# Kernel tuning notes

Hardware: AMD Instinct MI355X
Metric: run time of the kernel (lower is better)

Reference implementation:

```python
import jax, jax.numpy as jnp
import numpy as np

NUM_HEADS = 14
SCALE = 0.125  # fixed constant in the source, not 1/sqrt(head_dim)
PATCH = 14
DIM = 3 * PATCH * PATCH  # 588


def setup_inputs() -> dict:
    key = jax.random.key(0)
    k_x, k_cw, k_cb, k_qw, k_qb = jax.random.split(key, 5)
    B, C_in, H, W = 8, 3, 448, 448
    x = jax.random.normal(k_x, (B, C_in, H, W), dtype=jnp.float32)
    # Conv2d(in_channels=3, dim, kernel=patch, stride=patch), torch layout OIHW
    fan_in = C_in * PATCH * PATCH
    bound = 1.0 / np.sqrt(fan_in)
    conv_w = jax.random.uniform(k_cw, (DIM, C_in, PATCH, PATCH), jnp.float32, -bound, bound)
    conv_b = jax.random.uniform(k_cb, (DIM,), jnp.float32, -bound, bound)
    # Linear(dim, 3*dim): weight [out, in] torch layout
    lb = 1.0 / np.sqrt(DIM)
    qkv_w = jax.random.uniform(k_qw, (3 * DIM, DIM), jnp.float32, -lb, lb)
    qkv_b = jax.random.uniform(k_qb, (3 * DIM,), jnp.float32, -lb, lb)
    return {"x": x, "conv_w": conv_w, "conv_b": conv_b, "qkv_w": qkv_w, "qkv_b": qkv_b}


def reference(x, conv_w, conv_b, qkv_w, qkv_b):
    # Patch embedding: conv kernel==stride==patch  -> [B, DIM, H/p, W/p]
    y = jax.lax.conv_general_dilated(
        x, conv_w, window_strides=(PATCH, PATCH), padding="VALID",
        dimension_numbers=("NCHW", "OIHW", "NCHW"))
    y = y + conv_b[None, :, None, None]
    B = y.shape[0]
    # flatten(2).transpose(1, 2) -> [B, N, C]
    tokens = y.reshape(B, DIM, -1).transpose(0, 2, 1)
    N, C = tokens.shape[1], tokens.shape[2]
    hd = C // NUM_HEADS  # 42
    qkv = tokens @ qkv_w.T + qkv_b  # [B, N, 3C]
    qkv = qkv.reshape(B, N, 3, NUM_HEADS, hd).transpose(2, 0, 3, 1, 4)  # [3,B,H,N,hd]
    q, k, v = qkv[0], qkv[1], qkv[2]
    attn = jnp.einsum("bhnd,bhmd->bhnm", q, k) * SCALE  # [B,H,N,N]
    attn = jax.nn.softmax(attn, axis=-1)
    out = jnp.einsum("bhnm,bhmd->bhnd", attn, v)  # [B,H,N,hd]
    out = out.transpose(0, 2, 1, 3).reshape(B, N, C)  # [B,N,C]
    return out
```

## Files before the change

### kernel.cpp

```cpp
#include <hip/hip_runtime.h>

typedef unsigned short u16;
typedef unsigned int u32;
typedef unsigned long long u64;
typedef __attribute__((ext_vector_type(8))) short bf16x8;
typedef __attribute__((ext_vector_type(4))) float f32x4;

#define MTOK 8192
#define KP   640
#define CC   588
#define C3   1764
#define NH   14
#define SEQ  1024
#define HD   42
#define DP   64
#define DV   48
#define SC2f 0.18033688011112042f

static __device__ __forceinline__ u16 f2b(float f) {
  unsigned u = __builtin_bit_cast(unsigned, f);
  u = (u + 0x7FFFu + ((u >> 16) & 1u)) >> 16;
  return (u16)u;
}

static __device__ __forceinline__ void gl_lds16(const void* g, void* l) {
  auto gp = (const unsigned int __attribute__((address_space(1)))*)((unsigned long long)g);
  auto lp = (unsigned int __attribute__((address_space(3)))*)((unsigned long long)l);
  __builtin_amdgcn_global_load_lds(gp, lp, 16, 0, 0);
}

static __device__ __forceinline__ u32 pk2(float lo, float hi) {
  u32 a = __builtin_bit_cast(u32, lo) + 0x8000u;
  u32 b = __builtin_bit_cast(u32, hi) + 0x8000u;
  return __builtin_amdgcn_perm(b, a, 0x07060302u);
}

__global__ void im2col_k(const float* __restrict__ x, u16* __restrict__ A,
                         u16* __restrict__ vT, u16* __restrict__ kb) {
  int t = blockIdx.x;
  int b = t >> 10, pi = t & 1023, ph = pi >> 5, pw = pi & 31;
  const float* xb = x + (size_t)b * 3 * 448 * 448;
  for (int kk = threadIdx.x; kk < KP; kk += 256) {
    float v = 0.f;
    if (kk < CC) {
      int c = kk / 196, rem = kk - c * 196, i = rem / 14, j = rem - i * 14;
      v = xb[(size_t)(c * 448 + ph * 14 + i) * 448 + pw * 14 + j];
    }
    A[(size_t)t * KP + kk] = f2b(v);
  }
  if (t < 112) {
    u16* row = vT + ((size_t)(t * DV + HD)) * SEQ;
    for (int n = threadIdx.x; n < SEQ; n += 256) row[n] = 0x3F80;
    for (int n = threadIdx.x; n < SEQ; n += 256) {
      u64* p = (u64*)&kb[((size_t)t * SEQ + n) * DP + 40];
      p[0] = 0; p[1] = 0; p[2] = 0;
    }
  }
}

__global__ void padw_k(const float* __restrict__ wc, const float* __restrict__ wq,
                       u16* __restrict__ dc, u16* __restrict__ dq) {
  int r = blockIdx.x;
  const float* src; u16* dst; int R, rr;
  if (r < 640) { src = wc; dst = dc; R = CC; rr = r; }
  else         { src = wq; dst = dq; R = C3; rr = r - 640; }
  for (int c = threadIdx.x; c < KP; c += 256) {
    float v = (rr < R && c < CC) ? src[(size_t)rr * CC + c] : 0.f;
    dst[(size_t)rr * KP + c] = f2b(v);
  }
}

template <int MODE>
__global__ void __launch_bounds__(256, 2) gemm_k(
    const u16* __restrict__ A, const u16* __restrict__ Bt,
    const float* __restrict__ bias, u16* __restrict__ out0,
    u16* __restrict__ qb, u16* __restrict__ kb, u16* __restrict__ vb) {
  __shared__ alignas(16) u16 sA[128 * 64];
  __shared__ alignas(16) u16 sB[128 * 64];
  const int tid = threadIdx.x;
  const int wave = tid >> 6, lane = tid & 63, quad = lane >> 4, l16 = lane & 15;
  const int wi = wave >> 1, wj = wave & 1;
  const int m0 = blockIdx.x * 128, n0 = blockIdx.y * 128;
  const int rL = lane >> 3, scid = lane & 7;
  const f32x4 z4 = {0.f, 0.f, 0.f, 0.f};

  f32x4 acc[4][4];
#pragma unroll
  for (int i = 0; i < 4; i++)
#pragma unroll
    for (int j = 0; j < 4; j++) acc[i][j] = z4;

  for (int k0 = 0; k0 < KP; k0 += 64) {
    __syncthreads();
#pragma unroll
    for (int cc = wave; cc < 16; cc += 4) {
      int r = cc * 8 + rL;
      gl_lds16(A + ((size_t)(m0 + r) * KP + k0 + (scid ^ (r & 7)) * 8), &sA[cc * 512]);
    }
#pragma unroll
    for (int cc = wave; cc < 16; cc += 4) {
      int r = cc * 8 + rL;
      gl_lds16(Bt + ((size_t)(n0 + r) * KP + k0 + (scid ^ (r & 7)) * 8), &sB[cc * 512]);
    }
    __syncthreads();
#pragma unroll
    for (int ks = 0; ks < 2; ks++) {
      bf16x8 af[4], bfr[4];
#pragma unroll
      for (int i = 0; i < 4; i++) {
        int r = wi * 64 + i * 16 + l16;
        af[i] = *(const bf16x8*)&sA[r * 64 + (((ks * 4 + quad) ^ (r & 7)) * 8)];
      }
#pragma unroll
      for (int j = 0; j < 4; j++) {
        int r = wj * 64 + j * 16 + l16;
        bfr[j] = *(const bf16x8*)&sB[r * 64 + (((ks * 4 + quad) ^ (r & 7)) * 8)];
      }
#pragma unroll
      for (int i = 0; i < 4; i++)
#pragma unroll
        for (int j = 0; j < 4; j++)
          acc[i][j] = __builtin_amdgcn_mfma_f32_16x16x32_bf16(af[i], bfr[j], acc[i][j], 0, 0, 0);
    }
  }

  const int baser = wi * 64 + quad * 4;
  if (MODE == 0) {
#pragma unroll
    for (int j = 0; j < 4; j++) {
      int col = n0 + wj * 64 + j * 16 + l16;
      float bs = (col < CC) ? bias[col] : 0.f;
#pragma unroll
      for (int i = 0; i < 4; i++) {
        int row = m0 + baser + i * 16;
#pragma unroll
        for (int r = 0; r < 4; r++)
          out0[(size_t)(row + r) * KP + col] = f2b(acc[i][j][r] + bs);
      }
    }
  } else {
#pragma unroll
    for (int j = 0; j < 4; j++) {
      int col = n0 + wj * 64 + j * 16 + l16;
      if (col < C3) {
        float bs = bias[col];
        int which = col / CC;
        int rem = col - which * CC;
        int h = rem / HD;
        int d = rem - h * HD;
        if (which < 2) {
          u16* dst = (which == 0) ? qb : kb;
          float sc = (which == 0) ? SC2f : 1.0f;
#pragma unroll
          for (int i = 0; i < 4; i++) {
            int row = m0 + baser + i * 16;
#pragma unroll
            for (int r = 0; r < 4; r++) {
              int rw = row + r;
              int b = rw >> 10, n = rw & 1023;
              dst[((size_t)((b * NH + h) * SEQ + n)) * DP + d] = f2b((acc[i][j][r] + bs) * sc);
            }
          }
        } else {
#pragma unroll
          for (int i = 0; i < 4; i++) {
            int row = m0 + baser + i * 16;
            int b = row >> 10, n = row & 1023;
            u64 pk = (u64)f2b(acc[i][j][0] + bs) | ((u64)f2b(acc[i][j][1] + bs) << 16) |
                     ((u64)f2b(acc[i][j][2] + bs) << 32) | ((u64)f2b(acc[i][j][3] + bs) << 48);
            *(u64*)&vb[((size_t)((b * NH + h) * DV + d)) * SEQ + n] = pk;
          }
        }
      }
    }
  }
}

__global__ void __launch_bounds__(256) attn_k(
    const u16* __restrict__ qb, const u16* __restrict__ kb,
    const u16* __restrict__ vT, float* __restrict__ out) {
  __shared__ alignas(16) u16 sK[2][64 * 64];
  __shared__ alignas(16) u16 sV[2][DV * 64];
  __shared__ alignas(16) u16 sP[4][16 * 72];
  const int tid = threadIdx.x;
  const int wave = tid >> 6, lane = tid & 63, quad = lane >> 4, l16 = lane & 15;
  const int g = blockIdx.x;
  const int bh = (g & 7) * 14 + (g >> 7);
  const int qt = (g >> 3) & 15;
  const int q0 = qt * 64;
  const int rL = lane >> 3, scid = lane & 7;
  const f32x4 z4 = {0.f, 0.f, 0.f, 0.f};
  u16* sPw = sP[wave];

  bf16x8 aq0, aq1;
  {
    const u16* qrow = qb + ((size_t)(bh * SEQ + q0 + wave * 16 + l16)) * DP;
    aq0 = *(const bf16x8*)&qrow[quad * 8];
    aq1 = *(const bf16x8*)&qrow[32 + quad * 8];
  }
  f32x4 o[3] = {z4, z4, z4};

  const u16* kb0 = kb + (size_t)bh * SEQ * DP;
  const u16* vb0 = vT + (size_t)bh * DV * SEQ;

#define STAGE(bufi, m0_)                                                                    \
  {                                                                                         \
    _Pragma("unroll") for (int cc = wave; cc < 8; cc += 4) {                                \
      int r = cc * 8 + rL;                                                                  \
      gl_lds16(kb0 + ((size_t)((m0_) + r)) * DP + (scid ^ ((r >> 2) & 7)) * 8,              \
               &sK[bufi][cc * 512]);                                                        \
    }                                                                                       \
    _Pragma("unroll") for (int cc = wave; cc < 6; cc += 4) {                                \
      int d = cc * 8 + rL;                                                                  \
      gl_lds16(vb0 + (size_t)d * SEQ + (m0_) + (scid ^ (d & 7)) * 8, &sV[bufi][cc * 512]);  \
    }                                                                                       \
  }

  STAGE(0, 0);

  for (int kt = 0; kt < 16; kt++) {
    __syncthreads();
    if (kt < 15) STAGE((kt + 1) & 1, (kt + 1) * 64);
    const u16* sKb = sK[kt & 1];
    const u16* sVb = sV[kt & 1];
    bf16x8 bk[4][2];
#pragma unroll
    for (int j = 0; j < 4; j++) {
      int rr = 4 * l16 + j;
#pragma unroll
      for (int ks = 0; ks < 2; ks++)
        bk[j][ks] = *(const bf16x8*)&sKb[rr * 64 + (((ks * 4 + quad) ^ (l16 & 7)) * 8)];
    }
    f32x4 s[4];
#pragma unroll
    for (int j = 0; j < 4; j++) {
      f32x4 t = __builtin_amdgcn_mfma_f32_16x16x32_bf16(aq0, bk[j][0], z4, 0, 0, 0);
      s[j] = __builtin_amdgcn_mfma_f32_16x16x32_bf16(aq1, bk[j][1], t, 0, 0, 0);
    }
#pragma unroll
    for (int r = 0; r < 4; r++) {
      u32 d0 = pk2(__builtin_amdgcn_exp2f(s[0][r]), __builtin_amdgcn_exp2f(s[1][r]));
      u32 d1 = pk2(__builtin_amdgcn_exp2f(s[2][r]), __builtin_amdgcn_exp2f(s[3][r]));
      u32* dst = (u32*)&sPw[(quad * 4 + r) * 72 + l16 * 4];
      dst[0] = d0;
      dst[1] = d1;
    }
#pragma unroll
    for (int ks = 0; ks < 2; ks++) {
      bf16x8 ap = *(const bf16x8*)&sPw[l16 * 72 + ks * 32 + quad * 8];
#pragma unroll
      for (int j = 0; j < 3; j++) {
        int d = j * 16 + l16;
        bf16x8 bv = *(const bf16x8*)&sVb[d * 64 + (((ks * 4 + quad) ^ (d & 7)) * 8)];
        o[j] = __builtin_amdgcn_mfma_f32_16x16x32_bf16(ap, bv, o[j], 0, 0, 0);
      }
    }
  }
#undef STAGE

  const int b = bh / NH, h = bh - b * NH;
#pragma unroll
  for (int r = 0; r < 4; r++) {
    float ls = __shfl(o[2][r], (lane & 48) + 10, 64);
    float rc = 1.f / ls;
    int row = wave * 16 + quad * 4 + r;
    float* orow = out + ((size_t)(b * SEQ + q0 + row)) * CC + h * HD;
#pragma unroll
    for (int j = 0; j < 3; j++) {
      int d = j * 16 + l16;
      if (d < HD) orow[d] = o[j][r] * rc;
    }
  }
}

extern "C" void kernel_launch(void* const* d_in, const int* in_sizes, int n_in,
                              void* d_out, int out_size, void* d_ws, size_t ws_size,
                              hipStream_t stream) {
  (void)in_sizes; (void)n_in; (void)out_size; (void)ws_size;
  const float* x      = (const float*)d_in[0];
  const float* conv_w = (const float*)d_in[1];
  const float* conv_b = (const float*)d_in[2];
  const float* qkv_w  = (const float*)d_in[3];
  const float* qkv_b  = (const float*)d_in[4];
  float* out = (float*)d_out;

  char* ws = (char*)d_ws;
  size_t off = 0;
  u16* A      = (u16*)(ws + off); off += (size_t)MTOK * KP * 2;
  u16* Wc     = (u16*)(ws + off); off += (size_t)640 * KP * 2;
  u16* Wq     = (u16*)(ws + off); off += (size_t)1792 * KP * 2;
  u16* tokens = (u16*)(ws + off); off += (size_t)MTOK * KP * 2;
  u16* qbuf   = (u16*)(ws + off); off += (size_t)112 * SEQ * DP * 2;
  u16* kbuf   = (u16*)(ws + off); off += (size_t)112 * SEQ * DP * 2;
  u16* vTb    = (u16*)(ws + off); off += (size_t)112 * DV * SEQ * 2;

  im2col_k<<<MTOK, 256, 0, stream>>>(x, A, vTb, kbuf);
  padw_k<<<2432, 256, 0, stream>>>(conv_w, qkv_w, Wc, Wq);
  gemm_k<0><<<dim3(64, 5), 256, 0, stream>>>(A, Wc, conv_b, tokens, nullptr, nullptr, nullptr);
  gemm_k<1><<<dim3(64, 14), 256, 0, stream>>>(tokens, Wq, qkv_b, nullptr, qbuf, kbuf, vTb);
  attn_k<<<1792, 256, 0, stream>>>(qbuf, kbuf, vTb, out);
}
```

Measured before the change: 174.1 us.

## Fold patch-embedding conv weights into QKV projection to drop one token GEMM

Precomputes a fused weight Wf = Wq·Wc and fused bias (Wq·cb + qb) with a small weight-only GEMM, so the activations go through one GEMM instead of two (8192x640x640 conv GEMM eliminated). Also vectorizes the im2col bf16 packing, zeroes padding of q as well as k, and clamps the exp2 argument. The cost is an extra small weight GEMM each call and a different rounding path, since the fused weights are rounded to bf16 once rather than rounding the intermediate tokens.

New measurement: 188.3 us. 1.08x slower.

```diff
diff --git a/kernel.cpp b/kernel.cpp
--- a/kernel.cpp
+++ b/kernel.cpp
@@ -36,37 +36,51 @@
 }
 
 __global__ void im2col_k(const float* __restrict__ x, u16* __restrict__ A,
-                         u16* __restrict__ vT, u16* __restrict__ kb) {
+                         u16* __restrict__ vT, u16* __restrict__ qb, u16* __restrict__ kb) {
   int t = blockIdx.x;
   int b = t >> 10, pi = t & 1023, ph = pi >> 5, pw = pi & 31;
   const float* xb = x + (size_t)b * 3 * 448 * 448;
-  for (int kk = threadIdx.x; kk < KP; kk += 256) {
-    float v = 0.f;
+  u32* Arow = (u32*)(A + (size_t)t * KP);
+  for (int h = threadIdx.x; h < KP / 2; h += 256) {
+    int kk = h * 2;
+    u32 v = 0;
     if (kk < CC) {
       int c = kk / 196, rem = kk - c * 196, i = rem / 14, j = rem - i * 14;
-      v = xb[(size_t)(c * 448 + ph * 14 + i) * 448 + pw * 14 + j];
-    }
-    A[(size_t)t * KP + kk] = f2b(v);
+      const float* p = &xb[(size_t)(c * 448 + ph * 14 + i) * 448 + pw * 14 + j];
+      v = pk2(p[0], p[1]);
+    }
+    Arow[h] = v;
   }
   if (t < 112) {
     u16* row = vT + ((size_t)(t * DV + HD)) * SEQ;
     for (int n = threadIdx.x; n < SEQ; n += 256) row[n] = 0x3F80;
     for (int n = threadIdx.x; n < SEQ; n += 256) {
-      u64* p = (u64*)&kb[((size_t)t * SEQ + n) * DP + 40];
-      p[0] = 0; p[1] = 0; p[2] = 0;
-    }
-  }
-}
-
-__global__ void padw_k(const float* __restrict__ wc, const float* __restrict__ wq,
-                       u16* __restrict__ dc, u16* __restrict__ dq) {
+      u64* pq = (u64*)&qb[((size_t)t * SEQ + n) * DP + 40];
+      u64* pk = (u64*)&kb[((size_t)t * SEQ + n) * DP + 40];
+#pragma unroll
+      for (int z = 0; z < 3; z++) { pq[z] = 0; pk[z] = 0; }
+    }
+  }
+}
+
+__global__ void padw_k(const float* __restrict__ wq, const float* __restrict__ wc,
+                       const float* __restrict__ cb, u16* __restrict__ dq, u16* __restrict__ dct) {
   int r = blockIdx.x;
-  const float* src; u16* dst; int R, rr;
-  if (r < 640) { src = wc; dst = dc; R = CC; rr = r; }
-  else         { src = wq; dst = dq; R = C3; rr = r - 640; }
-  for (int c = threadIdx.x; c < KP; c += 256) {
-    float v = (rr < R && c < CC) ? src[(size_t)rr * CC + c] : 0.f;
-    dst[(size_t)rr * KP + c] = f2b(v);
+  if (r < 1792) {
+    for (int c = threadIdx.x; c < KP; c += 256) {
+      float v = (r < C3 && c < CC) ? wq[(size_t)r * CC + c] : 0.f;
+      dq[(size_t)r * KP + c] = f2b(v);
+    }
+  } else {
+    int i = r - 1792;
+    for (int c = threadIdx.x; c < KP; c += 256) {
+      float v = 0.f;
+      if (c < CC) {
+        if (i < CC) v = wc[(size_t)c * CC + i];
+        else if (i == CC) v = cb[c];
+      }
+      dct[(size_t)i * KP + c] = f2b(v);
+    }
   }
 }
 
@@ -74,7 +88,8 @@
 __global__ void __launch_bounds__(256, 2) gemm_k(
     const u16* __restrict__ A, const u16* __restrict__ Bt,
     const float* __restrict__ bias, u16* __restrict__ out0,
-    u16* __restrict__ qb, u16* __restrict__ kb, u16* __restrict__ vb) {
+    u16* __restrict__ qb, u16* __restrict__ kb, u16* __restrict__ vb,
+    float* __restrict__ bf) {
   __shared__ alignas(16) u16 sA[128 * 64];
   __shared__ alignas(16) u16 sB[128 * 64];
   const int tid = threadIdx.x;
@@ -129,13 +144,14 @@
 #pragma unroll
     for (int j = 0; j < 4; j++) {
       int col = n0 + wj * 64 + j * 16 + l16;
-      float bs = (col < CC) ? bias[col] : 0.f;
 #pragma unroll
       for (int i = 0; i < 4; i++) {
         int row = m0 + baser + i * 16;
 #pragma unroll
-        for (int r = 0; r < 4; r++)
-          out0[(size_t)(row + r) * KP + col] = f2b(acc[i][j][r] + bs);
+        for (int r = 0; r < 4; r++) {
+          out0[(size_t)(row + r) * KP + col] = f2b(acc[i][j][r]);
+          if (col == CC && row + r < C3) bf[row + r] = bias[row + r] + acc[i][j][r];
+        }
       }
     }
   } else {
@@ -239,11 +255,13 @@
     }
 #pragma unroll
     for (int r = 0; r < 4; r++) {
-      u32 d0 = pk2(__builtin_amdgcn_exp2f(s[0][r]), __builtin_amdgcn_exp2f(s[1][r]));
-      u32 d1 = pk2(__builtin_amdgcn_exp2f(s[2][r]), __builtin_amdgcn_exp2f(s[3][r]));
+      float e0 = __builtin_amdgcn_exp2f(fminf(s[0][r], 64.f));
+      float e1 = __builtin_amdgcn_exp2f(fminf(s[1][r], 64.f));
+      float e2 = __builtin_amdgcn_exp2f(fminf(s[2][r], 64.f));
+      float e3 = __builtin_amdgcn_exp2f(fminf(s[3][r], 64.f));
       u32* dst = (u32*)&sPw[(quad * 4 + r) * 72 + l16 * 4];
-      dst[0] = d0;
-      dst[1] = d1;
+      dst[0] = pk2(e0, e1);
+      dst[1] = pk2(e2, e3);
     }
 #pragma unroll
     for (int ks = 0; ks < 2; ks++) {
@@ -287,16 +305,18 @@
   char* ws = (char*)d_ws;
   size_t off = 0;
   u16* A      = (u16*)(ws + off); off += (size_t)MTOK * KP * 2;
-  u16* Wc     = (u16*)(ws + off); off += (size_t)640 * KP * 2;
   u16* Wq     = (u16*)(ws + off); off += (size_t)1792 * KP * 2;
-  u16* tokens = (u16*)(ws + off); off += (size_t)MTOK * KP * 2;
+  u16* WcT    = (u16*)(ws + off); off += (size_t)640 * KP * 2;
+  u16* Wf     = (u16*)(ws + off); off += (size_t)1792 * KP * 2;
+  float* bfus = (float*)(ws + off); off += (size_t)C3 * 4;
+  off = (off + 255) & ~(size_t)255;
   u16* qbuf   = (u16*)(ws + off); off += (size_t)112 * SEQ * DP * 2;
   u16* kbuf   = (u16*)(ws + off); off += (size_t)112 * SEQ * DP * 2;
   u16* vTb    = (u16*)(ws + off); off += (size_t)112 * DV * SEQ * 2;
 
-  im2col_k<<<MTOK, 256, 0, stream>>>(x, A, vTb, kbuf);
-  padw_k<<<2432, 256, 0, stream>>>(conv_w, qkv_w, Wc, Wq);
-  gemm_k<0><<<dim3(64, 5), 256, 0, stream>>>(A, Wc, conv_b, tokens, nullptr, nullptr, nullptr);
-  gemm_k<1><<<dim3(64, 14), 256, 0, stream>>>(tokens, Wq, qkv_b, nullptr, qbuf, kbuf, vTb);
+  im2col_k<<<MTOK, 256, 0, stream>>>(x, A, vTb, qbuf, kbuf);
+  padw_k<<<2432, 256, 0, stream>>>(qkv_w, conv_w, conv_b, Wq, WcT);
+  gemm_k<0><<<dim3(14, 5), 256, 0, stream>>>(Wq, WcT, qkv_b, Wf, nullptr, nullptr, nullptr, bfus);
+  gemm_k<1><<<dim3(64, 14), 256, 0, stream>>>(A, Wf, bfus, nullptr, qbuf, kbuf, vTb, nullptr);
   attn_k<<<1792, 256, 0, stream>>>(qbuf, kbuf, vTb, out);
 }
```
